# Performance work log

Measured on AMD Instinct MI355X. Metric: run time of the kernel, lower is better.

The kernel has to match this reference:

```python
import jax, jax.numpy as jnp
import numpy as np

# Config matching init_kwargs: dim=256, input_resolution=(64,64), num_heads=8,
# stride=2, dynamic_factor=2, window_size=8, Attention_Group=2, postype='rel', k=None
DIM, H, W = 256, 64, 64
HEADS, HG, STRIDE, WS, FACTOR = 8, 2, 2, 8, 2.0
GC = DIM // HG                 # channels per attention group (offset net width)
HC = DIM // HEADS              # per-head channels
RH, RW = H // STRIDE, W // STRIDE
WH, WW = H // WS, W // WS
B = 2
MLP_HID = 4 * DIM
EPS = 1e-5


def _grid_sample(img, grid):
    # img: (N, C, H, W); grid: (N, Hg, Wg, 2) with (row, col) in [-1, 1].
    # Bilinear, align_corners=True, zero padding (matches F.grid_sample).
    N, C, Hi, Wi = img.shape
    rows = (grid[..., 0] + 1.0) * 0.5 * (Hi - 1)
    cols = (grid[..., 1] + 1.0) * 0.5 * (Wi - 1)
    r0f = jnp.floor(rows); c0f = jnp.floor(cols)
    wr = rows - r0f; wc = cols - c0f
    r0 = r0f.astype(jnp.int32); c0 = c0f.astype(jnp.int32)

    def gather(ri, ci):
        valid = ((ri >= 0) & (ri < Hi) & (ci >= 0) & (ci < Wi)).astype(img.dtype)
        rc = jnp.clip(ri, 0, Hi - 1); cc = jnp.clip(ci, 0, Wi - 1)
        vals = jax.vmap(lambda im, r, c: im[:, r, c])(img, rc, cc)  # (N, C, Hg, Wg)
        return vals * valid[:, None]

    return (gather(r0, c0) * ((1 - wr) * (1 - wc))[:, None]
            + gather(r0, c0 + 1) * ((1 - wr) * wc)[:, None]
            + gather(r0 + 1, c0) * (wr * (1 - wc))[:, None]
            + gather(r0 + 1, c0 + 1) * (wr * wc)[:, None])


def _ln2d(z, g, b):
    mu = jnp.mean(z, axis=1, keepdims=True)
    var = jnp.var(z, axis=1, keepdims=True)
    return (z - mu) * jax.lax.rsqrt(var + EPS) * g[None, :, None, None] + b[None, :, None, None]


def _conv1x1(z, w, b=None):
    out = jnp.einsum('oc,bchw->bohw', w, z)
    return out if b is None else out + b[None, :, None, None]


def _forward(x, ln1_g, ln1_b, q_w, q_b, k_w, k_b, v_w, v_b,
             off1_w, off2_w, off3_w, bn_g, bn_b, bn_m, bn_v, off4_w,
             posembed, proj_w, proj_b, ln2_g, ln2_b,
             mlp_w1, mlp_b1, mlp_w2, mlp_b2):
    Bx, C = x.shape[0], x.shape[1]
    R, NW, WT = RH * RW, WH * WW, WS * WS
    scale = C ** -0.5  # original uses dim**-0.5 (not head_dim) as default qk scale

    xa = _ln2d(x, ln1_g, ln1_b)
    q = _conv1x1(xa, q_w, q_b)

    # ---- per-group offset prediction: 3 depthwise strided convs -> BN -> GELU -> 1x1 ----
    qg = q.reshape(Bx * HG, GC, H, W)

    def dw(z, w):
        return jax.lax.conv_general_dilated(z, w, (2, 2), ((1, 1), (1, 1)),
                feature_group_count=GC, dimension_numbers=('NCHW', 'OIHW', 'NCHW'))

    o = dw(dw(dw(qg, off1_w), off2_w), off3_w)  # (B*HG, GC, WH, WW)
    o = (o - bn_m[None, :, None, None]) * jax.lax.rsqrt(bn_v + EPS)[None, :, None, None]
    o = o * bn_g[None, :, None, None] + bn_b[None, :, None, None]
    o = jax.nn.gelu(o, approximate=False)
    off = jnp.einsum('oc,bchw->bohw', off4_w, o)               # (B*HG, 2R, WH, WW)
    off = off.reshape(Bx * HG, 2, R, NW).transpose(0, 3, 2, 1)  # (B*HG, NW, R, 2)
    ranges = jnp.array([1.0 / H, 1.0 / W], dtype=x.dtype)
    off = jnp.tanh(off) * ranges * FACTOR

    # ---- reference points normalized to [-1, 1] (align_corners=True convention) ----
    ref_r = (jnp.arange(RH, dtype=x.dtype) * STRIDE) / (H - 1) * 2.0 - 1.0
    ref_c = (jnp.arange(RW, dtype=x.dtype) * STRIDE) / (W - 1) * 2.0 - 1.0
    ref = jnp.stack(jnp.meshgrid(ref_r, ref_c, indexing='ij'), axis=-1).reshape(R, 2)
    grid = off + ref[None, None]                                # (B*HG, NW, R, 2)

    # ---- deformable gather of values at predicted sample locations ----
    value = xa.reshape(Bx * HG, GC, H, W)
    samp = _grid_sample(value, grid).reshape(Bx, C, NW, R)

    kk = _conv1x1(samp, k_w, k_b).reshape(Bx * HEADS, HC, NW, R).transpose(0, 2, 1, 3)
    vv = _conv1x1(samp, v_w, v_b).reshape(Bx * HEADS, HC, NW, R).transpose(0, 2, 1, 3)

    # ---- windowed queries ----
    wq = q.reshape(Bx * HEADS, HC, H, W).transpose(0, 2, 3, 1)
    wq = wq.reshape(Bx * HEADS, WH, WS, WW, WS, HC).transpose(0, 1, 3, 2, 4, 5)
    wq = wq.reshape(Bx * HEADS, NW, WT, HC) * scale

    attn = jnp.einsum('nwqc,nwcr->nwqr', wq, kk)                # (B*h, NW, WT, R)

    # ---- relative position bias: query pixel vs. (stride-spaced) reference point ----
    rel_y = (jnp.arange(RH) * STRIDE)[None, :] - jnp.arange(H)[:, None] + (H - 1)  # (H, RH)
    rel_x = (jnp.arange(RW) * STRIDE)[None, :] - jnp.arange(W)[:, None] + (W - 1)  # (W, RW)
    t = posembed[:, rel_y, :]                                   # (h, H, RH, 2W-1)
    bias = t[:, :, :, rel_x]                                    # (h, H, RH, W, RW)
    bias = bias.transpose(0, 1, 3, 2, 4).reshape(HEADS, H, W, R)
    bias = bias.reshape(HEADS, WH, WS, WW, WS, R).transpose(0, 1, 3, 2, 4, 5)
    bias = bias.reshape(HEADS, NW, WT, R)

    attn = attn.reshape(Bx, HEADS, NW, WT, R) + bias[None]
    attn = jax.nn.softmax(attn, axis=-1).reshape(Bx * HEADS, NW, WT, R)
    out = jnp.einsum('nwqr,nwcr->nwqc', attn, vv)               # (B*h, NW, WT, HC)
    out = out.reshape(Bx * HEADS, WH, WW, WS, WS, HC).transpose(0, 1, 3, 2, 4, 5)
    out = out.reshape(Bx, HEADS, H, W, HC).transpose(0, 1, 4, 2, 3).reshape(Bx, C, H, W)
    out = _conv1x1(out, proj_w, proj_b)

    x = x + out
    xm = _ln2d(x, ln2_g, ln2_b)
    hdn = jax.nn.gelu(_conv1x1(xm, mlp_w1, mlp_b1), approximate=False)
    return x + _conv1x1(hdn, mlp_w2, mlp_b2)


def setup_inputs() -> dict:
    key = jax.random.key(0)
    ks = jax.random.split(key, 16)
    f32 = jnp.float32

    def n(k, shape, std=0.02):
        return jax.random.normal(k, shape, dtype=f32) * std

    R = RH * RW
    return {
        'x': jax.random.normal(ks[0], (B, DIM, H, W), dtype=f32),
        'ln1_g': jnp.ones((DIM,), f32), 'ln1_b': jnp.zeros((DIM,), f32),
        'q_w': n(ks[1], (DIM, DIM)), 'q_b': jnp.zeros((DIM,), f32),
        'k_w': n(ks[2], (DIM, DIM)), 'k_b': jnp.zeros((DIM,), f32),
        'v_w': n(ks[3], (DIM, DIM)), 'v_b': jnp.zeros((DIM,), f32),
        'off1_w': n(ks[4], (GC, 1, 3, 3)),
        'off2_w': n(ks[5], (GC, 1, 3, 3)),
        'off3_w': n(ks[6], (GC, 1, 3, 3)),
        'bn_g': jnp.ones((GC,), f32), 'bn_b': jnp.zeros((GC,), f32),
        'bn_m': jnp.zeros((GC,), f32), 'bn_v': jnp.ones((GC,), f32),
        'off4_w': n(ks[7], (2 * R, GC)),
        'posembed': n(ks[8], (HEADS, 2 * H - 1, 2 * W - 1), std=0.01),
        'proj_w': n(ks[9], (DIM, DIM)), 'proj_b': jnp.zeros((DIM,), f32),
        'ln2_g': jnp.ones((DIM,), f32), 'ln2_b': jnp.zeros((DIM,), f32),
        'mlp_w1': n(ks[10], (MLP_HID, DIM)), 'mlp_b1': jnp.zeros((MLP_HID,), f32),
        'mlp_w2': n(ks[11], (DIM, MLP_HID)), 'mlp_b2': jnp.zeros((DIM,), f32),
    }


def reference(x, ln1_g, ln1_b, q_w, q_b, k_w, k_b, v_w, v_b,
              off1_w, off2_w, off3_w, bn_g, bn_b, bn_m, bn_v, off4_w,
              posembed, proj_w, proj_b, ln2_g, ln2_b,
              mlp_w1, mlp_b1, mlp_w2, mlp_b2):
    return _forward(x, ln1_g, ln1_b, q_w, q_b, k_w, k_b, v_w, v_b,
                    off1_w, off2_w, off3_w, bn_g, bn_b, bn_m, bn_v, off4_w,
                    posembed, proj_w, proj_b, ln2_g, ln2_b,
                    mlp_w1, mlp_b1, mlp_w2, mlp_b2)
```

## Files before the change

### kernel.cpp

```cpp
#include <hip/hip_runtime.h>
#include <hip/hip_bf16.h>
#include <math.h>


typedef __hip_bfloat16 bf16;
typedef __bf16 bf16x8 __attribute__((ext_vector_type(8)));
typedef float f32x4 __attribute__((ext_vector_type(4)));

union U16x8 { uint4 u4; unsigned short us[8]; };

__device__ __forceinline__ float cvt(float x) { return x; }
__device__ __forceinline__ float cvt(bf16 x) { return __bfloat162float(x); }
__device__ __forceinline__ float b2f(unsigned short u) {
  union { float f; unsigned int v; } x; x.v = ((unsigned int)u) << 16; return x.f;
}
__device__ __forceinline__ unsigned short f2b(float f) {
  bf16 h = __float2bfloat16(f);
  return *reinterpret_cast<unsigned short*>(&h);
}
__device__ __forceinline__ float gelu_f(float x) {
  return 0.5f * x * (1.0f + erff(x * 0.7071067811865475f));
}
__device__ __forceinline__ void stout(float* p, float v) { *p = v; }
__device__ __forceinline__ void stout(bf16* p, float v) { *p = __float2bfloat16(v); }

__global__ __launch_bounds__(256) void setup_kernel(
    const float* __restrict__ x, const float* __restrict__ g,
    const float* __restrict__ bta,
    const float* __restrict__ q_w, const float* __restrict__ q_b,
    const float* __restrict__ k_w, const float* __restrict__ v_w,
    const float* __restrict__ pjw, const float* __restrict__ w1,
    const float* __restrict__ w2, const float* __restrict__ off4w,
    bf16* __restrict__ out, float* __restrict__ xnhwc,
    unsigned short* __restrict__ wqkv, float* __restrict__ bqkv,
    unsigned short* __restrict__ wproj, unsigned short* __restrict__ wmlp1,
    unsigned short* __restrict__ wmlp2, unsigned short* __restrict__ woff4i)
{
  __shared__ float s1[8][32], s2[8][32];
  __shared__ unsigned short tb[32][264];
  int bid = blockIdx.x;
  int t = threadIdx.x;
  if (bid < 256) {
    int pos = t & 31, cs = t >> 5;
    int p = bid * 32 + pos;
    int bb = p >> 12, hw = p & 4095;
    const float* xp = x + (size_t)bb * 256 * 4096 + hw;
    float vloc[32];
    float sum = 0.f, ss = 0.f;
#pragma unroll
    for (int i = 0; i < 32; ++i) {
      float v = xp[(size_t)(cs * 32 + i) * 4096];
      vloc[i] = v; sum += v; ss += v * v;
    }
    s1[cs][pos] = sum; s2[cs][pos] = ss;
    {
      float* xo = xnhwc + (size_t)p * 256 + cs * 32;
#pragma unroll
      for (int qd = 0; qd < 8; ++qd)
        *(float4*)(xo + qd * 4) = make_float4(vloc[qd*4], vloc[qd*4+1],
                                              vloc[qd*4+2], vloc[qd*4+3]);
    }
    __syncthreads();
    if (cs == 0) {
      float S = 0.f, Q = 0.f;
#pragma unroll
      for (int i = 0; i < 8; ++i) { S += s1[i][pos]; Q += s2[i][pos]; }
      float mu = S * (1.f / 256.f);
      float var = Q * (1.f / 256.f) - mu * mu;
      s1[0][pos] = mu;
      s2[0][pos] = rsqrtf(var + 1e-5f);
    }
    __syncthreads();
    float mu = s1[0][pos], rs = s2[0][pos];
#pragma unroll
    for (int i = 0; i < 32; ++i) {
      int c = cs * 32 + i;
      tb[pos][c] = f2b((vloc[i] - mu) * rs * g[c] + bta[c]);
    }
    __syncthreads();
    int px = t >> 3, grp = t & 7;
    bf16* op = out + ((size_t)bid * 32 + px) * 256 + grp * 32;
#pragma unroll
    for (int q = 0; q < 4; ++q)
      *(uint4*)(op + q * 8) = *(const uint4*)&tb[px][grp * 32 + q * 8];
  } else {
    int idx = (bid - 256) * 256 + t;
    const int S0 = 1280 * 256;
    const int S1 = S0 + 1280;
    const int S2 = S1 + 256 * 256;
    const int S3 = S2 + 1024 * 256;
    const int S4 = S3 + 256 * 1024;
    const int S5 = S4 + 2048 * 128;
    if (idx < S0) {
      int n = idx >> 8, c = idx & 255;
      float v;
      if (n < 256)       v = q_w[n * 256 + c];
      else if (n < 512)  v = (c < 128)  ? k_w[(n - 256) * 256 + c] : 0.f;
      else if (n < 768)  v = (c >= 128) ? k_w[(n - 512) * 256 + c] : 0.f;
      else if (n < 1024) v = (c < 128)  ? v_w[(n - 768) * 256 + c] : 0.f;
      else               v = (c >= 128) ? v_w[(n - 1024) * 256 + c] : 0.f;
      wqkv[idx] = f2b(v);
    } else if (idx < S1) {
      int n = idx - S0;
      bqkv[n] = (n < 256) ? q_b[n] : 0.f;
    } else if (idx < S2) {
      wproj[idx - S1] = f2b(pjw[idx - S1]);
    } else if (idx < S3) {
      wmlp1[idx - S2] = f2b(w1[idx - S2]);
    } else if (idx < S4) {
      wmlp2[idx - S3] = f2b(w2[idx - S3]);
    } else if (idx < S5) {
      int kk = idx - S4;
      int n = kk >> 7, c = kk & 127;
      woff4i[kk] = f2b(off4w[((size_t)((n & 1) * 1024 + (n >> 1))) * 128 + c]);
    }
  }
}

__global__ __launch_bounds__(256) void ln2_kernel(
    const bf16* __restrict__ xin, const float* __restrict__ g,
    const float* __restrict__ bta, bf16* __restrict__ out)
{
  __shared__ float sa[8][32], sb[8][32];
  __shared__ float mu_s[32], rs_s[32];
  int t = threadIdx.x;
  int px = t >> 3, grp = t & 7;
  size_t p = (size_t)blockIdx.x * 32 + px;
  const bf16* xp = xin + p * 256 + grp * 32;
  float v[32]; float sum = 0.f, ss = 0.f;
#pragma unroll
  for (int q = 0; q < 4; ++q) {
    U16x8 u; u.u4 = *(const uint4*)(xp + q * 8);
#pragma unroll
    for (int j = 0; j < 8; ++j) {
      float f = b2f(u.us[j]); v[q * 8 + j] = f; sum += f; ss += f * f;
    }
  }
  sa[grp][px] = sum; sb[grp][px] = ss;
  __syncthreads();
  if (t < 32) {
    float S = 0.f, Q = 0.f;
#pragma unroll
    for (int i = 0; i < 8; ++i) { S += sa[i][t]; Q += sb[i][t]; }
    float mu = S * (1.f / 256.f);
    mu_s[t] = mu;
    rs_s[t] = rsqrtf(Q * (1.f / 256.f) - mu * mu + 1e-5f);
  }
  __syncthreads();
  float mu = mu_s[px], rs = rs_s[px];
  bf16* op = out + p * 256 + grp * 32;
#pragma unroll
  for (int q = 0; q < 4; ++q) {
    U16x8 o;
#pragma unroll
    for (int j = 0; j < 8; ++j) {
      int c = grp * 32 + q * 8 + j;
      o.us[j] = f2b((v[q * 8 + j] - mu) * rs * g[c] + bta[c]);
    }
    *(uint4*)(op + q * 8) = o.u4;
  }
}

template<int OUTM, int RESM, int ACT, int BM>
__global__ __launch_bounds__(256) void mgemm_kernel(
    const bf16* __restrict__ A, const unsigned short* __restrict__ Bw,
    const float* __restrict__ bias, const void* __restrict__ res,
    void* __restrict__ out, int N, int K, int lda, int ldb)
{
  constexpr int MT = BM / 32;
  constexpr int AB_BYTES = (BM + 64) * 72 * 2;
  constexpr int T_LD = BM + 5;
  constexpr int T_BYTES = 64 * T_LD * 4;
  constexpr int SH_BYTES = (OUTM == 1 && T_BYTES > AB_BYTES) ? T_BYTES : AB_BYTES;
  __shared__ __attribute__((aligned(16))) char shraw[SH_BYTES];
  auto As = reinterpret_cast<unsigned short(*)[72]>(shraw);
  auto Bs = reinterpret_cast<unsigned short(*)[72]>(shraw + BM * 72 * 2);
  float (*T)[T_LD] = reinterpret_cast<float(*)[T_LD]>(shraw);

  int t = threadIdx.x;
  int m0 = blockIdx.y * BM, n0 = blockIdx.x * 64;
  int lane = t & 63, w = t >> 6;
  int l15 = lane & 15, quad = lane >> 4;
  int wm = (w >> 1) * (BM / 2), wn = (w & 1) * 32;
  f32x4 acc[MT][2];
#pragma unroll
  for (int mt = 0; mt < MT; ++mt)
#pragma unroll
    for (int nt = 0; nt < 2; ++nt) acc[mt][nt] = (f32x4){0.f, 0.f, 0.f, 0.f};

  for (int k0 = 0; k0 < K; k0 += 64) {
#pragma unroll
    for (int i = 0; i < MT; ++i) {
      int idx = t + i * 256;
      int m = idx >> 3, oc = (idx & 7) * 8;
      *(uint4*)&As[m][oc] = *(const uint4*)(A + (size_t)(m0 + m) * lda + k0 + oc);
    }
#pragma unroll
    for (int i = 0; i < 2; ++i) {
      int idx = t + i * 256;
      int n = idx >> 3, oc = (idx & 7) * 8;
      *(uint4*)&Bs[n][oc] = *(const uint4*)(Bw + (size_t)(n0 + n) * ldb + k0 + oc);
    }
    __syncthreads();
#pragma unroll
    for (int ks = 0; ks < 2; ++ks) {
      bf16x8 af[MT], bfr[2];
#pragma unroll
      for (int mt = 0; mt < MT; ++mt)
        af[mt] = __builtin_bit_cast(bf16x8,
            *(const uint4*)&As[wm + mt * 16 + l15][ks * 32 + quad * 8]);
#pragma unroll
      for (int nt = 0; nt < 2; ++nt)
        bfr[nt] = __builtin_bit_cast(bf16x8,
            *(const uint4*)&Bs[wn + nt * 16 + l15][ks * 32 + quad * 8]);
#pragma unroll
      for (int mt = 0; mt < MT; ++mt)
#pragma unroll
        for (int nt = 0; nt < 2; ++nt)
          acc[mt][nt] = __builtin_amdgcn_mfma_f32_16x16x32_bf16(
              af[mt], bfr[nt], acc[mt][nt], 0, 0, 0);
    }
    __syncthreads();
  }
  float bv[2];
#pragma unroll
  for (int nt = 0; nt < 2; ++nt)
    bv[nt] = bias ? bias[n0 + wn + nt * 16 + l15] : 0.f;
#pragma unroll
  for (int mt = 0; mt < MT; ++mt) {
#pragma unroll
    for (int nt = 0; nt < 2; ++nt) {
#pragma unroll
      for (int reg = 0; reg < 4; ++reg) {
        int m = m0 + wm + mt * 16 + quad * 4 + reg;
        int n = n0 + wn + nt * 16 + l15;
        float v = acc[mt][nt][reg] + bv[nt];
        if constexpr (ACT == 1) v = gelu_f(v);
        if constexpr (RESM == 1)
          v += ((const float*)res)[(size_t)m * N + n];
        if constexpr (RESM == 2)
          v += b2f(((const unsigned short*)res)[(size_t)m * N + n]);
        if constexpr (OUTM == 0)
          ((unsigned short*)out)[(size_t)m * N + n] = f2b(v);
        if constexpr (OUTM == 1)
          T[(n - n0)][(m - m0)] = v;
        if constexpr (OUTM == 4)
          ((unsigned short*)out)[((size_t)(n >> 8) * 8192 + m) * 256 + (n & 255)] = f2b(v);
        if constexpr (OUTM == 5) {
          float val = tanhf(v) * (2.0f / 64.0f);
          int r = n >> 1, coord = n & 1;
          int rc = coord ? (r & 31) : (r >> 5);
          float ref = rc * (4.0f / 63.0f) - 1.0f;
          float pix = (val + ref + 1.0f) * 31.5f;
          float other = __shfl_xor(pix, 1, 64);
          if (coord == 0) {
            float rowp = pix, colp = other;
            float r0f = floorf(rowp), c0f = floorf(colp);
            float wr = rowp - r0f, wc = colp - c0f;
            int r0 = (int)r0f, c0 = (int)c0f;
            bool rv0 = ((unsigned)r0 < 64u), rv1 = ((unsigned)(r0 + 1) < 64u);
            bool cv0 = ((unsigned)c0 < 64u), cv1 = ((unsigned)(c0 + 1) < 64u);
            float4 w4;
            w4.x = (rv0 && cv0) ? (1.f - wr) * (1.f - wc) : 0.f;
            w4.y = (rv0 && cv1) ? (1.f - wr) * wc : 0.f;
            w4.z = (rv1 && cv0) ? wr * (1.f - wc) : 0.f;
            w4.w = (rv1 && cv1) ? wr * wc : 0.f;
            ((int*)out)[(size_t)m * 1024 + r] = r0 * 64 + c0;
            *(float4*)((float*)res + ((size_t)m * 1024 + r) * 4) = w4;
          }
        }
      }
    }
  }
  if constexpr (OUTM == 1) {
    __syncthreads();
    constexpr int SEGS = BM / 32;
    int units = 64 * SEGS;
    if (t < units) {
      int nl = t / SEGS, seg = t % SEGS;
      int bI = m0 >> 12, hw0 = m0 & 4095;
      float* op = (float*)out + ((size_t)bI * 256 + n0 + nl) * 4096 + hw0 + seg * 32;
#pragma unroll
      for (int k = 0; k < 32; ++k) op[k] = T[nl][seg * 32 + k];
    }
  }
}

template<typename TI, typename TO, int IC>
__global__ __launch_bounds__(256) void dwconv_kernel(
    const TI* __restrict__ in, const float* __restrict__ wgt,
    TO* __restrict__ out, int Hi, int Wi, int Ho, int Wo, int fuse,
    const float* __restrict__ bg_, const float* __restrict__ bb_,
    const float* __restrict__ bm_, const float* __restrict__ bv_)
{
  int idx = blockIdx.x * 256 + threadIdx.x;
  int c = idx & 127;
  int pp = idx >> 7;
  int ow = pp % Wo, oh = (pp / Wo) % Ho, bgi = pp / (Wo * Ho);
  const TI* ip;
  if constexpr (IC == 256)
    ip = in + ((size_t)(bgi >> 1) * 4096) * 256 + (bgi & 1) * 128 + c;
  else
    ip = in + ((size_t)bgi * Hi * Wi) * 128 + c;
  float acc = 0.f;
#pragma unroll
  for (int ky = 0; ky < 3; ++ky) {
    int ih = oh * 2 - 1 + ky;
    if ((unsigned)ih >= (unsigned)Hi) continue;
#pragma unroll
    for (int kx = 0; kx < 3; ++kx) {
      int iw = ow * 2 - 1 + kx;
      if ((unsigned)iw >= (unsigned)Wi) continue;
      acc += wgt[c * 9 + ky * 3 + kx] * cvt(ip[(size_t)(ih * Wi + iw) * IC]);
    }
  }
  if (fuse) {
    acc = (acc - bm_[c]) * rsqrtf(bv_[c] + 1e-5f) * bg_[c] + bb_[c];
    acc = gelu_f(acc);
  }
  stout(out + idx, acc);
}

__device__ __forceinline__ void gather_issue(
    int rc0, int b, int nw, int gr_r, int choff,
    const int* __restrict__ goff, const float* __restrict__ gwt,
    const unsigned short* __restrict__ Kimg, const unsigned short* __restrict__ Vimg,
    uint4* kc, uint4* vc, f32x4* wv)
{
#pragma unroll
  for (int g = 0; g < 2; ++g) {
    size_t cbase = ((size_t)(b * 2 + g) * 64 + nw) * 1024 + rc0 + gr_r;
    int base = goff[cbase];
    wv[g] = *(const f32x4*)(gwt + cbase * 4);
    int o00 = min(max(base, 0), 4095);
    int o01 = min(max(base + 1, 0), 4095);
    int o10 = min(max(base + 64, 0), 4095);
    int o11 = min(max(base + 65, 0), 4095);
    size_t pb = ((size_t)g * 8192 + (size_t)b * 4096) * 256 + choff;
    kc[g * 4 + 0] = *(const uint4*)(Kimg + pb + (size_t)o00 * 256);
    vc[g * 4 + 0] = *(const uint4*)(Vimg + pb + (size_t)o00 * 256);
    kc[g * 4 + 1] = *(const uint4*)(Kimg + pb + (size_t)o01 * 256);
    vc[g * 4 + 1] = *(const uint4*)(Vimg + pb + (size_t)o01 * 256);
    kc[g * 4 + 2] = *(const uint4*)(Kimg + pb + (size_t)o10 * 256);
    vc[g * 4 + 2] = *(const uint4*)(Vimg + pb + (size_t)o10 * 256);
    kc[g * 4 + 3] = *(const uint4*)(Kimg + pb + (size_t)o11 * 256);
    vc[g * 4 + 3] = *(const uint4*)(Vimg + pb + (size_t)o11 * 256);
  }
}

__global__ __launch_bounds__(256) void gather_kernel(
    const unsigned short* __restrict__ Kimg, const unsigned short* __restrict__ Vimg,
    const int* __restrict__ goff, const float* __restrict__ gwt,
    unsigned short* __restrict__ Ks, unsigned short* __restrict__ Vs)
{
  int t = threadIdx.x;
  int pos = blockIdx.x * 8 + (t >> 5);
  int oct = t & 31;
  int r = pos & 1023;
  int nw = (pos >> 10) & 63;
  int b = pos >> 16;
  int ch0 = oct * 8;

  uint4 kc[8], vc[8];
  f32x4 wv[2];
  gather_issue(r, b, nw, 0, ch0, goff, gwt, Kimg, Vimg, kc, vc, wv);

  float aK[8] = {0,0,0,0,0,0,0,0}, aV[8] = {0,0,0,0,0,0,0,0};
#pragma unroll
  for (int g = 0; g < 2; ++g)
#pragma unroll
    for (int c4 = 0; c4 < 4; ++c4) {
      U16x8 ku, vu; ku.u4 = kc[g * 4 + c4]; vu.u4 = vc[g * 4 + c4];
      float wvv = wv[g][c4];
#pragma unroll
      for (int j = 0; j < 8; ++j) { aK[j] += wvv * b2f(ku.us[j]); aV[j] += wvv * b2f(vu.us[j]); }
    }
  U16x8 ok, ov;
#pragma unroll
  for (int j = 0; j < 8; ++j) { ok.us[j] = f2b(aK[j]); ov.us[j] = f2b(aV[j]); }
  int head = oct >> 2, chh = (oct & 3) * 8;
  size_t obase = (((size_t)(b * 8 + head) * 64 + nw) * 1024 + r) * 32 + chh;
  *(uint4*)(Ks + obase) = ok.u4;
  *(uint4*)(Vs + obase) = ov.u4;
}

__global__ __launch_bounds__(256) void attn2_kernel(
    const bf16* __restrict__ qbuf, const unsigned short* __restrict__ Ks,
    const unsigned short* __restrict__ Vs, const float* __restrict__ vbv,
    const float* __restrict__ pe, bf16* __restrict__ aout)
{
  __shared__ unsigned short vs[2][32][72];
  __shared__ unsigned short PsQs[64][72];
  __shared__ unsigned short pesb[70][72];

  int blk = blockIdx.x;
  int b = blk & 1, head = (blk >> 1) & 7, nw = blk >> 4;
  int wh = nw >> 3, ww = nw & 7;
  int t = threadIdx.x;
  int lane = t & 63, w = t >> 6;
  int l15 = lane & 15, quad = lane >> 4;
  int qc0 = head * 32;
  int vr = t >> 2, vseg = t & 3;

  size_t kvbase = ((size_t)(b * 8 + head) * 64 + nw) * 1024 * 32;
  const unsigned short* Kb = Ks + kvbase;
  const unsigned short* Vb = Vs + kvbase;

  {
    int qt = t >> 2, oct = t & 3;
    int h = wh * 8 + (qt >> 3), wcol = ww * 8 + (qt & 7);
    const bf16* src = qbuf + ((size_t)b * 4096 + h * 64 + wcol) * 256 + qc0 + oct * 8;
    U16x8 u; u.u4 = *(const uint4*)src;
    U16x8 o;
#pragma unroll
    for (int j = 0; j < 8; ++j) o.us[j] = f2b(b2f(u.us[j]) * 0.0625f);
    *(uint4*)&PsQs[qt][oct * 8] = o.u4;
  }
  int ry0 = 56 - wh * 8, rx0 = 56 - ww * 8;
  for (int i = t; i < 70 * 70; i += 256) {
    int yy = i / 70, xx = i % 70;
    pesb[yy][xx] = f2b(pe[(size_t)head * 16129 + (ry0 + yy) * 127 + rx0 + xx]);
  }
  {
    U16x8 vu; vu.u4 = *(const uint4*)(Vb + (size_t)t * 8);
#pragma unroll
    for (int j = 0; j < 8; ++j) {
      int row = vseg * 8 + j;
      vs[0][row][vr ^ (((row >> 3) & 3) * 8)] = vu.us[j];
    }
  }
  uint4 kf[4];
#pragma unroll
  for (int nt = 0; nt < 4; ++nt)
    kf[nt] = *(const uint4*)(Kb + (size_t)(nt * 16 + l15) * 32 + quad * 8);
  __syncthreads();

  bf16x8 aQ = __builtin_bit_cast(bf16x8, *(const uint4*)&PsQs[w * 16 + l15][quad * 8]);
  float l[4] = {0.f, 0.f, 0.f, 0.f};
  f32x4 oacc[2];
  oacc[0] = (f32x4){0.f, 0.f, 0.f, 0.f};
  oacc[1] = (f32x4){0.f, 0.f, 0.f, 0.f};

  uint4 vcn = make_uint4(0u, 0u, 0u, 0u);
  uint4 kfn[4];
  for (int c = 0; c < 16; ++c) {
    int cur = c & 1, rc0 = c * 64;
    if (c) {
      U16x8 vu; vu.u4 = vcn;
#pragma unroll
      for (int j = 0; j < 8; ++j) {
        int row = vseg * 8 + j;
        vs[cur][row][vr ^ (((row >> 3) & 3) * 8)] = vu.us[j];
      }
      __syncthreads();
    }
    if (c < 15) {
      size_t nb = (size_t)(rc0 + 64) * 32;
      vcn = *(const uint4*)(Vb + nb + (size_t)t * 8);
#pragma unroll
      for (int nt = 0; nt < 4; ++nt)
        kfn[nt] = *(const uint4*)(Kb + nb + (size_t)(nt * 16 + l15) * 32 + quad * 8);
    }

    f32x4 s[4];
#pragma unroll
    for (int nt = 0; nt < 4; ++nt) {
      bf16x8 bK = __builtin_bit_cast(bf16x8, kf[nt]);
      f32x4 z = (f32x4){0.f, 0.f, 0.f, 0.f};
      s[nt] = __builtin_amdgcn_mfma_f32_16x16x32_bf16(aQ, bK, z, 0, 0, 0);
    }
#pragma unroll
    for (int nt = 0; nt < 4; ++nt) {
      int rg_ = nt * 16 + l15;
      int rrow = (rc0 + rg_) >> 5, rcol = rg_ & 31;
#pragma unroll
      for (int reg = 0; reg < 4; ++reg) {
        int q = w * 16 + quad * 4 + reg;
        s[nt][reg] += b2f(pesb[2 * rrow + 7 - (q >> 3)][2 * rcol + 7 - (q & 7)]);
      }
    }
#pragma unroll
    for (int reg = 0; reg < 4; ++reg) {
      float ps = 0.f;
#pragma unroll
      for (int nt = 0; nt < 4; ++nt) {
        float p = __expf(s[nt][reg]);
        PsQs[w * 16 + quad * 4 + reg][nt * 16 + l15] = f2b(p);
        ps += p;
      }
      ps += __shfl_xor(ps, 1, 64);
      ps += __shfl_xor(ps, 2, 64);
      ps += __shfl_xor(ps, 4, 64);
      ps += __shfl_xor(ps, 8, 64);
      l[reg] += ps;
    }
#pragma unroll
    for (int kst = 0; kst < 2; ++kst) {
      uint4 up = *(const uint4*)&PsQs[w * 16 + l15][kst * 32 + quad * 8];
      bf16x8 pA = __builtin_bit_cast(bf16x8, up);
#pragma unroll
      for (int nt2 = 0; nt2 < 2; ++nt2) {
        int row = nt2 * 16 + l15;
        int cbase = (kst * 32 + quad * 8) ^ (((row >> 3) & 3) * 8);
        uint4 uv = *(const uint4*)&vs[cur][row][cbase];
        bf16x8 vB = __builtin_bit_cast(bf16x8, uv);
        oacc[nt2] = __builtin_amdgcn_mfma_f32_16x16x32_bf16(pA, vB, oacc[nt2], 0, 0, 0);
      }
    }
    if (c < 15) {
#pragma unroll
      for (int nt = 0; nt < 4; ++nt) kf[nt] = kfn[nt];
    }
  }
#pragma unroll
  for (int nt2 = 0; nt2 < 2; ++nt2) {
    float vbias = vbv[qc0 + nt2 * 16 + l15];
#pragma unroll
    for (int reg = 0; reg < 4; ++reg) {
      int q = w * 16 + quad * 4 + reg;
      size_t p = (size_t)b * 4096 + (wh * 8 + (q >> 3)) * 64 + ww * 8 + (q & 7);
      aout[p * 256 + qc0 + nt2 * 16 + l15] =
          __float2bfloat16(oacc[nt2][reg] / l[reg] + vbias);
    }
  }
}

__global__ __launch_bounds__(256) void attn_kernel(
    const bf16* __restrict__ qbuf, const unsigned short* __restrict__ Kimg,
    const unsigned short* __restrict__ Vimg, const int* __restrict__ goff,
    const float* __restrict__ gwt, const float* __restrict__ vbv,
    const float* __restrict__ pe, bf16* __restrict__ aout)
{
  __shared__ unsigned short ks[2][64][40];
  __shared__ unsigned short vs[2][32][72];
  __shared__ unsigned short PsQs[64][72];
  __shared__ unsigned short pesb[70][72];

  int blk = blockIdx.x;
  int b = blk & 1, head = (blk >> 1) & 7, nw = blk >> 4;
  int wh = nw >> 3, ww = nw & 7;
  int t = threadIdx.x;
  int lane = t & 63, w = t >> 6;
  int l15 = lane & 15, quad = lane >> 4;
  int qc0 = head * 32;
  int gr_r = t >> 2, gr_seg = t & 3;
  int choff = qc0 + gr_seg * 8;

  {
    int qt = t >> 2, oct = t & 3;
    int h = wh * 8 + (qt >> 3), wcol = ww * 8 + (qt & 7);
    const bf16* src = qbuf + ((size_t)b * 4096 + h * 64 + wcol) * 256 + qc0 + oct * 8;
    U16x8 u; u.u4 = *(const uint4*)src;
    U16x8 o;
#pragma unroll
    for (int j = 0; j < 8; ++j) o.us[j] = f2b(b2f(u.us[j]) * 0.0625f);
    *(uint4*)&PsQs[qt][oct * 8] = o.u4;
  }
  int ry0 = 56 - wh * 8, rx0 = 56 - ww * 8;
  for (int i = t; i < 70 * 70; i += 256) {
    int yy = i / 70, xx = i % 70;
    pesb[yy][xx] = f2b(pe[(size_t)head * 16129 + (ry0 + yy) * 127 + rx0 + xx]);
  }

  uint4 kc[8], vc[8];
  f32x4 wv[2];
  gather_issue(0, b, nw, gr_r, choff, goff, gwt, Kimg, Vimg, kc, vc, wv);
  {
    float aK[8] = {0,0,0,0,0,0,0,0}, aV[8] = {0,0,0,0,0,0,0,0};
#pragma unroll
    for (int g = 0; g < 2; ++g)
#pragma unroll
      for (int c4 = 0; c4 < 4; ++c4) {
        U16x8 ku, vu; ku.u4 = kc[g * 4 + c4]; vu.u4 = vc[g * 4 + c4];
        float wvv = wv[g][c4];
#pragma unroll
        for (int j = 0; j < 8; ++j) { aK[j] += wvv * b2f(ku.us[j]); aV[j] += wvv * b2f(vu.us[j]); }
      }
    U16x8 ok;
#pragma unroll
    for (int j = 0; j < 8; ++j) ok.us[j] = f2b(aK[j]);
    *(uint4*)&ks[0][gr_r][gr_seg * 8] = ok.u4;
#pragma unroll
    for (int j = 0; j < 8; ++j) {
      int row = gr_seg * 8 + j;
      vs[0][row][gr_r ^ (((row >> 3) & 3) * 8)] = f2b(aV[j]);
    }
  }
  __syncthreads();

  bf16x8 aQ;
  {
    uint4 u = *(const uint4*)&PsQs[w * 16 + l15][quad * 8];
    aQ = __builtin_bit_cast(bf16x8, u);
  }
  float l[4] = {0.f, 0.f, 0.f, 0.f};
  f32x4 oacc[2];
  oacc[0] = (f32x4){0.f, 0.f, 0.f, 0.f};
  oacc[1] = (f32x4){0.f, 0.f, 0.f, 0.f};

  for (int c = 0; c < 16; ++c) {
    if (c) __syncthreads();
    int cur = c & 1, rc0 = c * 64;
    if (c < 15)
      gather_issue(rc0 + 64, b, nw, gr_r, choff, goff, gwt, Kimg, Vimg, kc, vc, wv);

    f32x4 s[4];
#pragma unroll
    for (int nt = 0; nt < 4; ++nt) {
      uint4 u = *(const uint4*)&ks[cur][nt * 16 + l15][quad * 8];
      bf16x8 bK = __builtin_bit_cast(bf16x8, u);
      f32x4 z = (f32x4){0.f, 0.f, 0.f, 0.f};
      s[nt] = __builtin_amdgcn_mfma_f32_16x16x32_bf16(aQ, bK, z, 0, 0, 0);
    }
#pragma unroll
    for (int nt = 0; nt < 4; ++nt) {
      int rg_ = nt * 16 + l15;
      int rrow = (rc0 + rg_) >> 5, rcol = rg_ & 31;
#pragma unroll
      for (int reg = 0; reg < 4; ++reg) {
        int q = w * 16 + quad * 4 + reg;
        s[nt][reg] += b2f(pesb[2 * rrow + 7 - (q >> 3)][2 * rcol + 7 - (q & 7)]);
      }
    }
#pragma unroll
    for (int reg = 0; reg < 4; ++reg) {
      float ps = 0.f;
#pragma unroll
      for (int nt = 0; nt < 4; ++nt) {
        float p = __expf(s[nt][reg]);
        PsQs[w * 16 + quad * 4 + reg][nt * 16 + l15] = f2b(p);
        ps += p;
      }
      ps += __shfl_xor(ps, 1, 64);
      ps += __shfl_xor(ps, 2, 64);
      ps += __shfl_xor(ps, 4, 64);
      ps += __shfl_xor(ps, 8, 64);
      l[reg] += ps;
    }
#pragma unroll
    for (int kst = 0; kst < 2; ++kst) {
      uint4 up = *(const uint4*)&PsQs[w * 16 + l15][kst * 32 + quad * 8];
      bf16x8 pA = __builtin_bit_cast(bf16x8, up);
#pragma unroll
      for (int nt2 = 0; nt2 < 2; ++nt2) {
        int row = nt2 * 16 + l15;
        int cbase = (kst * 32 + quad * 8) ^ (((row >> 3) & 3) * 8);
        uint4 uv = *(const uint4*)&vs[cur][row][cbase];
        bf16x8 vB = __builtin_bit_cast(bf16x8, uv);
        oacc[nt2] = __builtin_amdgcn_mfma_f32_16x16x32_bf16(pA, vB, oacc[nt2], 0, 0, 0);
      }
    }
    if (c < 15) {
      float aK[8] = {0,0,0,0,0,0,0,0}, aV[8] = {0,0,0,0,0,0,0,0};
#pragma unroll
      for (int g = 0; g < 2; ++g)
#pragma unroll
        for (int c4 = 0; c4 < 4; ++c4) {
          U16x8 ku, vu; ku.u4 = kc[g * 4 + c4]; vu.u4 = vc[g * 4 + c4];
          float wvv = wv[g][c4];
#pragma unroll
          for (int j = 0; j < 8; ++j) { aK[j] += wvv * b2f(ku.us[j]); aV[j] += wvv * b2f(vu.us[j]); }
        }
      int nxt = cur ^ 1;
      U16x8 ok;
#pragma unroll
      for (int j = 0; j < 8; ++j) ok.us[j] = f2b(aK[j]);
      *(uint4*)&ks[nxt][gr_r][gr_seg * 8] = ok.u4;
#pragma unroll
      for (int j = 0; j < 8; ++j) {
        int row = gr_seg * 8 + j;
        vs[nxt][row][gr_r ^ (((row >> 3) & 3) * 8)] = f2b(aV[j]);
      }
    }
  }
#pragma unroll
  for (int nt2 = 0; nt2 < 2; ++nt2) {
    float vbias = vbv[qc0 + nt2 * 16 + l15];
#pragma unroll
    for (int reg = 0; reg < 4; ++reg) {
      int q = w * 16 + quad * 4 + reg;
      size_t p = (size_t)b * 4096 + (wh * 8 + (q >> 3)) * 64 + ww * 8 + (q & 7);
      aout[p * 256 + qc0 + nt2 * 16 + l15] =
          __float2bfloat16(oacc[nt2][reg] / l[reg] + vbias);
    }
  }
}

extern "C" void kernel_launch(void* const* d_in, const int* in_sizes, int n_in,
                              void* d_out, int out_size, void* d_ws, size_t ws_size,
                              hipStream_t stream) {
  (void)in_sizes; (void)n_in; (void)out_size;
  const float* x     = (const float*)d_in[0];
  const float* ln1g  = (const float*)d_in[1];
  const float* ln1b  = (const float*)d_in[2];
  const float* q_w   = (const float*)d_in[3];
  const float* q_b   = (const float*)d_in[4];
  const float* k_w   = (const float*)d_in[5];
  const float* k_b   = (const float*)d_in[6];
  const float* v_w   = (const float*)d_in[7];
  const float* v_b   = (const float*)d_in[8];
  const float* off1w = (const float*)d_in[9];
  const float* off2w = (const float*)d_in[10];
  const float* off3w = (const float*)d_in[11];
  const float* bng   = (const float*)d_in[12];
  const float* bnb   = (const float*)d_in[13];
  const float* bnm   = (const float*)d_in[14];
  const float* bnv   = (const float*)d_in[15];
  const float* off4w = (const float*)d_in[16];
  const float* pe    = (const float*)d_in[17];
  const float* pjw   = (const float*)d_in[18];
  const float* pjb   = (const float*)d_in[19];
  const float* ln2g  = (const float*)d_in[20];
  const float* ln2b  = (const float*)d_in[21];
  const float* w1    = (const float*)d_in[22];
  const float* b1    = (const float*)d_in[23];
  const float* w2    = (const float*)d_in[24];
  const float* b2    = (const float*)d_in[25];
  (void)k_b;
  float* outp = (float*)d_out;

  char* W = (char*)d_ws;
  bf16*  xa    = (bf16*) (W + 0);
  float* dw1   = (float*)(W + 8388608);
  float* dw2   = (float*)(W + 10485760);
  bf16*  dw3b  = (bf16*) (W + 11010048);
  bf16*  qkv   = (bf16*) (W + 13238272);
  bf16*  qb    = qkv;
  bf16*  Kimg  = qkv + 2097152;
  bf16*  Vimg  = qkv + 3 * 2097152;
  bf16*  x2    = (bf16*) (W + 34209792);
  float* xnhwc = (float*)(W + 38404096);
  unsigned short* wqkv   = (unsigned short*)(W + 46792704);
  float*          bqkv   = (float*)         (W + 47448064);
  unsigned short* wproj  = (unsigned short*)(W + 47453184);
  unsigned short* wmlp1  = (unsigned short*)(W + 47584256);
  unsigned short* wmlp2  = (unsigned short*)(W + 48108544);
  unsigned short* woff4i = (unsigned short*)(W + 48632832);
  int*   goff  = (int*)  (W + 49157120);
  float* gwt   = (float*)(W + 50205696);
  unsigned short* Ksmp = (unsigned short*)(W + 54525952);
  unsigned short* Vsmp = (unsigned short*)(W + 121634816);
  const size_t WS_NEED = 188743680ull;
  bf16*  aout = xa;
  bf16*  xm   = xa;
  bf16*  hdn  = Kimg;

  setup_kernel<<<4869, 256, 0, stream>>>(
      x, ln1g, ln1b, q_w, q_b, k_w, v_w, pjw, w1, w2, off4w,
      xa, xnhwc, wqkv, bqkv, wproj, wmlp1, wmlp2, woff4i);
  mgemm_kernel<4, 0, 0, 128><<<dim3(20, 64), 256, 0, stream>>>(
      xa, wqkv, bqkv, nullptr, qkv, 1280, 256, 256, 256);
  dwconv_kernel<bf16, float, 256><<<2048, 256, 0, stream>>>(
      qb, off1w, dw1, 64, 64, 32, 32, 0, nullptr, nullptr, nullptr, nullptr);
  dwconv_kernel<float, float, 128><<<512, 256, 0, stream>>>(
      dw1, off2w, dw2, 32, 32, 16, 16, 0, nullptr, nullptr, nullptr, nullptr);
  dwconv_kernel<float, bf16, 128><<<128, 256, 0, stream>>>(
      dw2, off3w, dw3b, 16, 16, 8, 8, 1, bng, bnb, bnm, bnv);
  mgemm_kernel<5, 0, 0, 128><<<dim3(32, 2), 256, 0, stream>>>(
      dw3b, woff4i, nullptr, (const void*)gwt, goff, 2048, 128, 128, 128);
  if (ws_size >= WS_NEED) {
    gather_kernel<<<16384, 256, 0, stream>>>(
        (const unsigned short*)Kimg, (const unsigned short*)Vimg,
        goff, gwt, Ksmp, Vsmp);
    attn2_kernel<<<1024, 256, 0, stream>>>(
        qb, Ksmp, Vsmp, v_b, pe, aout);
  } else {
    attn_kernel<<<1024, 256, 0, stream>>>(
        qb, (const unsigned short*)Kimg, (const unsigned short*)Vimg,
        goff, gwt, v_b, pe, aout);
  }
  mgemm_kernel<0, 1, 0, 64><<<dim3(4, 128), 256, 0, stream>>>(
      aout, wproj, pjb, (const void*)xnhwc, x2, 256, 256, 256, 256);
  ln2_kernel<<<256, 256, 0, stream>>>(x2, ln2g, ln2b, xm);
  mgemm_kernel<0, 0, 1, 128><<<dim3(16, 64), 256, 0, stream>>>(
      xm, wmlp1, b1, nullptr, hdn, 1024, 256, 256, 256);
  mgemm_kernel<1, 2, 0, 64><<<dim3(4, 128), 256, 0, stream>>>(
      hdn, wmlp2, b2, (const void*)x2, outp, 256, 1024, 1024, 1024);
}
```

Measured before the change: 300.8 us.

## Split K/V gather into separate launches with block swizzle and nontemporal stores

The fused K/V gather kernel becomes a single-image gather kernel launched twice, once for K and once for V. It adds a block-index remap and writes its output with nontemporal stores, aiming for better cache locality of the source image and less cache pollution from the streaming output. In attention, the row-sum shuffle reduction moves out of the inner chunk loop to a single reduction at the end. The split reads the offsets and weights twice and adds one kernel launch.

```diff
diff --git a/kernel.cpp b/kernel.cpp
--- a/kernel.cpp
+++ b/kernel.cpp
@@ -6,8 +6,9 @@
 typedef __hip_bfloat16 bf16;
 typedef __bf16 bf16x8 __attribute__((ext_vector_type(8)));
 typedef float f32x4 __attribute__((ext_vector_type(4)));
-
-union U16x8 { uint4 u4; unsigned short us[8]; };
+typedef unsigned int u32x4 __attribute__((ext_vector_type(4)));
+
+union U16x8 { uint4 u4; u32x4 v4; unsigned short us[8]; };
 
 __device__ __forceinline__ float cvt(float x) { return x; }
 __device__ __forceinline__ float cvt(bf16 x) { return __bfloat162float(x); }
@@ -348,40 +349,51 @@
   }
 }
 
-__global__ __launch_bounds__(256) void gather_kernel(
-    const unsigned short* __restrict__ Kimg, const unsigned short* __restrict__ Vimg,
+__global__ __launch_bounds__(256) void gather1_kernel(
+    const unsigned short* __restrict__ img,
     const int* __restrict__ goff, const float* __restrict__ gwt,
-    unsigned short* __restrict__ Ks, unsigned short* __restrict__ Vs)
+    unsigned short* __restrict__ outp)
 {
+  int blk = blockIdx.x;
+  blk = (blk & 7) * 2048 + (blk >> 3);
   int t = threadIdx.x;
-  int pos = blockIdx.x * 8 + (t >> 5);
+  int pos = blk * 8 + (t >> 5);
   int oct = t & 31;
   int r = pos & 1023;
   int nw = (pos >> 10) & 63;
   int b = pos >> 16;
   int ch0 = oct * 8;
 
-  uint4 kc[8], vc[8];
-  f32x4 wv[2];
-  gather_issue(r, b, nw, 0, ch0, goff, gwt, Kimg, Vimg, kc, vc, wv);
-
-  float aK[8] = {0,0,0,0,0,0,0,0}, aV[8] = {0,0,0,0,0,0,0,0};
-#pragma unroll
-  for (int g = 0; g < 2; ++g)
+  float a[8] = {0.f, 0.f, 0.f, 0.f, 0.f, 0.f, 0.f, 0.f};
+#pragma unroll
+  for (int g = 0; g < 2; ++g) {
+    size_t cbase = ((size_t)(b * 2 + g) * 64 + nw) * 1024 + r;
+    int base = goff[cbase];
+    f32x4 wv = *(const f32x4*)(gwt + cbase * 4);
+    int o00 = min(max(base, 0), 4095);
+    int o01 = min(max(base + 1, 0), 4095);
+    int o10 = min(max(base + 64, 0), 4095);
+    int o11 = min(max(base + 65, 0), 4095);
+    size_t pb = ((size_t)g * 8192 + (size_t)b * 4096) * 256 + ch0;
+    uint4 cc[4];
+    cc[0] = *(const uint4*)(img + pb + (size_t)o00 * 256);
+    cc[1] = *(const uint4*)(img + pb + (size_t)o01 * 256);
+    cc[2] = *(const uint4*)(img + pb + (size_t)o10 * 256);
+    cc[3] = *(const uint4*)(img + pb + (size_t)o11 * 256);
 #pragma unroll
     for (int c4 = 0; c4 < 4; ++c4) {
-      U16x8 ku, vu; ku.u4 = kc[g * 4 + c4]; vu.u4 = vc[g * 4 + c4];
-      float wvv = wv[g][c4];
-#pragma unroll
-      for (int j = 0; j < 8; ++j) { aK[j] += wvv * b2f(ku.us[j]); aV[j] += wvv * b2f(vu.us[j]); }
-    }
-  U16x8 ok, ov;
-#pragma unroll
-  for (int j = 0; j < 8; ++j) { ok.us[j] = f2b(aK[j]); ov.us[j] = f2b(aV[j]); }
+      U16x8 u; u.u4 = cc[c4];
+      float wvv = wv[c4];
+#pragma unroll
+      for (int j = 0; j < 8; ++j) a[j] += wvv * b2f(u.us[j]);
+    }
+  }
+  U16x8 o;
+#pragma unroll
+  for (int j = 0; j < 8; ++j) o.us[j] = f2b(a[j]);
   int head = oct >> 2, chh = (oct & 3) * 8;
   size_t obase = (((size_t)(b * 8 + head) * 64 + nw) * 1024 + r) * 32 + chh;
-  *(uint4*)(Ks + obase) = ok.u4;
-  *(uint4*)(Vs + obase) = ov.u4;
+  __builtin_nontemporal_store(o.v4, (u32x4*)(outp + obase));
 }
 
 __global__ __launch_bounds__(256) void attn2_kernel(
@@ -488,10 +500,6 @@
         PsQs[w * 16 + quad * 4 + reg][nt * 16 + l15] = f2b(p);
         ps += p;
       }
-      ps += __shfl_xor(ps, 1, 64);
-      ps += __shfl_xor(ps, 2, 64);
-      ps += __shfl_xor(ps, 4, 64);
-      ps += __shfl_xor(ps, 8, 64);
       l[reg] += ps;
     }
 #pragma unroll
@@ -511,6 +519,13 @@
 #pragma unroll
       for (int nt = 0; nt < 4; ++nt) kf[nt] = kfn[nt];
     }
+  }
+#pragma unroll
+  for (int reg = 0; reg < 4; ++reg) {
+    l[reg] += __shfl_xor(l[reg], 1, 64);
+    l[reg] += __shfl_xor(l[reg], 2, 64);
+    l[reg] += __shfl_xor(l[reg], 4, 64);
+    l[reg] += __shfl_xor(l[reg], 8, 64);
   }
 #pragma unroll
   for (int nt2 = 0; nt2 < 2; ++nt2) {
@@ -759,9 +774,10 @@
   mgemm_kernel<5, 0, 0, 128><<<dim3(32, 2), 256, 0, stream>>>(
       dw3b, woff4i, nullptr, (const void*)gwt, goff, 2048, 128, 128, 128);
   if (ws_size >= WS_NEED) {
-    gather_kernel<<<16384, 256, 0, stream>>>(
-        (const unsigned short*)Kimg, (const unsigned short*)Vimg,
-        goff, gwt, Ksmp, Vsmp);
+    gather1_kernel<<<16384, 256, 0, stream>>>(
+        (const unsigned short*)Kimg, goff, gwt, Ksmp);
+    gather1_kernel<<<16384, 256, 0, stream>>>(
+        (const unsigned short*)Vimg, goff, gwt, Vsmp);
     attn2_kernel<<<1024, 256, 0, stream>>>(
         qb, Ksmp, Vsmp, v_b, pe, aout);
   } else {
```

Result: no change. 304.9 us (+1.3%).
